# Optimization experiments

Hardware: AMD Instinct MI355X
Metric: run time of the kernel (lower is better)

The kernel has to match this reference:

```python
import jax, jax.numpy as jnp
import numpy as np

N = 8192          # tokens
D_IN = 32768      # dec_input_size (SAE latent dim)
D_OUT = 768       # dec_hidden_size (model resid dim)


def setup_inputs() -> dict:
    key = jax.random.key(0)
    kx, kw = jax.random.split(key)
    x = jax.random.normal(kx, (N, D_IN), dtype=jnp.float32)
    W = jax.random.normal(kw, (D_OUT, D_IN), dtype=jnp.float32) * (1.0 / np.sqrt(D_IN))
    b_pre = jnp.zeros((D_IN,), dtype=jnp.float32)
    return {"x": x, "W": W, "b_pre": b_pre}


def reference(x, W, b_pre):
    # x: [N, D_in]; subtract pre-bias, then dense decode: (x - b_pre) @ W^T -> [N, D_out]
    x_adj = x - b_pre
    return jnp.einsum('nd,od->no', x_adj, W)
```

## Files before the change

kernel.cpp:

```cpp
#include <hip/hip_runtime.h>
#include <hip/hip_bf16.h>

#define TOK 8192
#define OUTD 768
#define KD 32768

#define BM 128
#define BN 768
#define BK 32
#define SPLITK 4
#define KCHUNK (KD / SPLITK)
#define NKT (KCHUNK / BK)
#define NHT_TOT (KD / BK)
#define THREADS 512
#define HTILE (BN * BK * 2)
#define ATILE (BM * BK * 2)

#define WSOFF_W 4096
#define WSOFF_P (WSOFF_W + (long)NHT_TOT * HTILE)
#define PSTRIDE ((long)TOK * OUTD)

typedef __attribute__((ext_vector_type(4))) float f32x4;
typedef __attribute__((ext_vector_type(16))) float f32x16;
typedef __attribute__((ext_vector_type(8))) short bf16x8;
typedef __attribute__((ext_vector_type(4))) unsigned int u32x4;

__device__ __forceinline__ unsigned pack2(float lo, float hi) {
    __hip_bfloat162 h = __float22bfloat162_rn(make_float2(lo, hi));
    unsigned u;
    __builtin_memcpy(&u, &h, 4);
    return u;
}

__device__ __forceinline__ u32x4 cvt_chunk(f32x4 a, f32x4 b) {
    u32x4 r;
    r[0] = pack2(a[0], a[1]);
    r[1] = pack2(a[2], a[3]);
    r[2] = pack2(b[0], b[1]);
    r[3] = pack2(b[2], b[3]);
    return r;
}

__global__ void colbias_kernel(const float* __restrict__ W,
                               const float* __restrict__ bp,
                               float* __restrict__ negc) {
    int o = blockIdx.x;
    int tid = threadIdx.x;
    const float* wr = W + (long)o * KD;
    float s = 0.f;
    for (int i = tid * 4; i < KD; i += 256 * 4) {
        f32x4 w = *(const f32x4*)(wr + i);
        f32x4 b = *(const f32x4*)(bp + i);
        s += w[0] * b[0] + w[1] * b[1] + w[2] * b[2] + w[3] * b[3];
    }
    #pragma unroll
    for (int off = 32; off > 0; off >>= 1) s += __shfl_down(s, off);
    __shared__ float red[4];
    if ((tid & 63) == 0) red[tid >> 6] = s;
    __syncthreads();
    if (tid == 0) negc[o] = -(red[0] + red[1] + red[2] + red[3]);
}

__global__ void cast_w_kernel(const float* __restrict__ W,
                              char* __restrict__ wsW) {
    int kth = blockIdx.x;
    int tid = threadIdx.x;
    int q = tid & 3;
    int c0 = tid >> 2;
    #pragma unroll
    for (int i = 0; i < 6; ++i) {
        int c = c0 + i * 128;
        const float* src = W + (long)c * KD + kth * 32 + q * 8;
        f32x4 a = ((const f32x4*)src)[0];
        f32x4 b = ((const f32x4*)src)[1];
        char* dst = wsW + (long)kth * HTILE + c * 64 + ((q ^ (c & 3)) << 4);
        *(u32x4*)dst = cvt_chunk(a, b);
    }
}

__global__ __launch_bounds__(THREADS, 2) void decoder_gemm(
    const float* __restrict__ X, const char* __restrict__ Wb16,
    float* __restrict__ P) {
    __shared__ char lds[2 * ATILE + 2 * HTILE];
    char* ldsA = lds;
    char* ldsB = lds + 2 * ATILE;

    const int bid = blockIdx.x;
    const int ks = bid & (SPLITK - 1);
    const int mt = bid >> 2;
    const int row0 = mt * BM;

    const int tid = threadIdx.x;
    const int lane = tid & 63;
    const int wid = tid >> 6;
    const int wm = wid >> 2;
    const int wn = wid & 3;
    const int l31 = lane & 31;
    const int hi = lane >> 5;

    const float* Xb = X + (long)row0 * KD + (long)ks * KCHUNK;
    const char* Wt0 = Wb16 + (long)ks * NKT * HTILE;

    const int ar = tid >> 2;
    const int aq = tid & 3;
    f32x4 xr[2];

    auto LOADA = [&](int kt) {
        const f32x4* p = (const f32x4*)(Xb + (long)ar * KD + kt * 32 + aq * 8);
        xr[0] = p[0];
        xr[1] = p[1];
    };

    const int asoff = ar * 64 + ((aq ^ (ar & 3)) << 4);

    auto STOREA = [&](int buf) {
        *(u32x4*)(ldsA + buf * ATILE + asoff) = cvt_chunk(xr[0], xr[1]);
    };

    auto ISSUEB = [&](int kt, int buf) {
        const char* src = Wt0 + (long)kt * HTILE + tid * 16;
        char* dst = ldsB + buf * HTILE + tid * 16;
        #pragma unroll
        for (int j = 0; j < 6; ++j)
            __builtin_amdgcn_global_load_lds(
                (const __attribute__((address_space(1))) void*)(src + j * 8192),
                (__attribute__((address_space(3))) void*)(dst + j * 8192),
                16, 0, 0);
    };

    int aoff[2], boff[6];
    #pragma unroll
    for (int m = 0; m < 2; ++m) {
        int row = wm * 64 + m * 32 + l31;
        aoff[m] = row * 64 + ((hi ^ (row & 3)) << 4);
    }
    #pragma unroll
    for (int n = 0; n < 6; ++n) {
        int col = wn * 192 + n * 32 + l31;
        boff[n] = col * 64 + ((hi ^ (col & 3)) << 4);
    }

    f32x16 acc[2][6];
    #pragma unroll
    for (int m = 0; m < 2; ++m)
        #pragma unroll
        for (int n = 0; n < 6; ++n)
            #pragma unroll
            for (int r = 0; r < 16; ++r) acc[m][n][r] = 0.f;

    auto COMPUTE = [&](int cur) {
        const char* As = ldsA + cur * ATILE;
        const char* Bs = ldsB + cur * HTILE;
        #pragma unroll
        for (int kk = 0; kk < 2; ++kk) {
            bf16x8 afr[2], bfr[6];
            #pragma unroll
            for (int m = 0; m < 2; ++m)
                afr[m] = *(const bf16x8*)(As + (aoff[m] ^ (kk << 5)));
            #pragma unroll
            for (int n = 0; n < 6; ++n)
                bfr[n] = *(const bf16x8*)(Bs + (boff[n] ^ (kk << 5)));
            __builtin_amdgcn_s_setprio(1);
            #pragma unroll
            for (int m = 0; m < 2; ++m)
                #pragma unroll
                for (int n = 0; n < 6; ++n)
                    acc[m][n] = __builtin_amdgcn_mfma_f32_32x32x16_bf16(
                        afr[m], bfr[n], acc[m][n], 0, 0, 0);
            __builtin_amdgcn_s_setprio(0);
        }
    };

    ISSUEB(0, 0);
    LOADA(0);
    STOREA(0);
    __syncthreads();

    for (int kt = 0; kt < NKT; ++kt) {
        const int cur = kt & 1;
        const bool more = (kt + 1 < NKT);
        if (more) {
            ISSUEB(kt + 1, cur ^ 1);
            LOADA(kt + 1);
        }
        COMPUTE(cur);
        if (more) STOREA(cur ^ 1);
        __syncthreads();
    }

    float* Pk = P + (long)ks * PSTRIDE;
    #pragma unroll
    for (int m = 0; m < 2; ++m) {
        int rowb = row0 + wm * 64 + m * 32 + 4 * hi;
        #pragma unroll
        for (int n = 0; n < 6; ++n) {
            int col = wn * 192 + n * 32 + l31;
            #pragma unroll
            for (int r = 0; r < 16; ++r) {
                int row = rowb + (r & 3) + 8 * (r >> 2);
                Pk[(long)row * OUTD + col] = acc[m][n][r];
            }
        }
    }
}

__global__ void reduce_kernel(const float* __restrict__ P,
                              const float* __restrict__ negc,
                              float* __restrict__ out) {
    long i4 = ((long)blockIdx.x * blockDim.x + threadIdx.x) * 4;
    int col = (int)(i4 % OUTD);
    f32x4 s = *(const f32x4*)(negc + col);
    #pragma unroll
    for (int ks = 0; ks < SPLITK; ++ks)
        s += *(const f32x4*)(P + ks * PSTRIDE + i4);
    *(f32x4*)(out + i4) = s;
}

extern "C" void kernel_launch(void* const* d_in, const int* in_sizes, int n_in,
                              void* d_out, int out_size, void* d_ws,
                              size_t ws_size, hipStream_t stream) {
    const float* x = (const float*)d_in[0];
    const float* W = (const float*)d_in[1];
    const float* bp = (const float*)d_in[2];
    float* out = (float*)d_out;
    float* negc = (float*)d_ws;
    char* wsW = (char*)d_ws + WSOFF_W;
    float* wsP = (float*)((char*)d_ws + WSOFF_P);

    hipLaunchKernelGGL(colbias_kernel, dim3(OUTD), dim3(256), 0, stream, W, bp,
                       negc);
    hipLaunchKernelGGL(cast_w_kernel, dim3(NHT_TOT), dim3(512), 0, stream, W,
                       wsW);
    hipLaunchKernelGGL(decoder_gemm, dim3((TOK / BM) * SPLITK), dim3(THREADS),
                       0, stream, x, wsW, wsP);
    hipLaunchKernelGGL(reduce_kernel, dim3((TOK * OUTD) / (256 * 4)), dim3(256),
                       0, stream, wsP, negc, out);
}
```

Measured before the change: 574.7 us.

## Triple-buffer W tiles with single A buffer and explicit vmcnt waits

Replaces the double-buffered A/B pipeline with a three-stage ring for the bf16 W tiles, prefetched two k-steps ahead, and a single LDS buffer for the converted X tile. Uses explicit s_waitcnt vmcnt(6) so the newest B prefetch can stay in flight across the barrier, plus a second barrier before each A store. The aim is to hide more global-to-LDS latency of the large W tile behind MFMA work. Launch bounds drop to 1 block per SM, which allows more registers but risks lower occupancy and an extra barrier per iteration.

```diff
diff --git a/kernel.cpp b/kernel.cpp
--- a/kernel.cpp
+++ b/kernel.cpp
@@ -78,12 +78,12 @@
     }
 }
 
-__global__ __launch_bounds__(THREADS, 2) void decoder_gemm(
+__global__ __launch_bounds__(THREADS, 1) void decoder_gemm(
     const float* __restrict__ X, const char* __restrict__ Wb16,
     float* __restrict__ P) {
-    __shared__ char lds[2 * ATILE + 2 * HTILE];
+    __shared__ char lds[ATILE + 3 * HTILE];
     char* ldsA = lds;
-    char* ldsB = lds + 2 * ATILE;
+    char* ldsB = lds + ATILE;
 
     const int bid = blockIdx.x;
     const int ks = bid & (SPLITK - 1);
@@ -113,8 +113,8 @@
 
     const int asoff = ar * 64 + ((aq ^ (ar & 3)) << 4);
 
-    auto STOREA = [&](int buf) {
-        *(u32x4*)(ldsA + buf * ATILE + asoff) = cvt_chunk(xr[0], xr[1]);
+    auto STOREA = [&]() {
+        *(u32x4*)(ldsA + asoff) = cvt_chunk(xr[0], xr[1]);
     };
 
     auto ISSUEB = [&](int kt, int buf) {
@@ -148,9 +148,9 @@
             #pragma unroll
             for (int r = 0; r < 16; ++r) acc[m][n][r] = 0.f;
 
-    auto COMPUTE = [&](int cur) {
-        const char* As = ldsA + cur * ATILE;
-        const char* Bs = ldsB + cur * HTILE;
+    auto COMPUTE = [&](int bbuf) {
+        const char* As = ldsA;
+        const char* Bs = ldsB + bbuf * HTILE;
         #pragma unroll
         for (int kk = 0; kk < 2; ++kk) {
             bf16x8 afr[2], bfr[6];
@@ -171,21 +171,27 @@
         }
     };
 
+    LOADA(0);
     ISSUEB(0, 0);
-    LOADA(0);
-    STOREA(0);
-    __syncthreads();
+    STOREA();
+    ISSUEB(1, 1);
+    asm volatile("s_waitcnt vmcnt(6) lgkmcnt(0)" ::: "memory");
+    __builtin_amdgcn_sched_barrier(0);
+    __builtin_amdgcn_s_barrier();
 
     for (int kt = 0; kt < NKT; ++kt) {
-        const int cur = kt & 1;
-        const bool more = (kt + 1 < NKT);
-        if (more) {
-            ISSUEB(kt + 1, cur ^ 1);
-            LOADA(kt + 1);
+        if (kt + 1 < NKT) LOADA(kt + 1);
+        if (kt + 2 < NKT) ISSUEB(kt + 2, (kt + 2) % 3);
+        COMPUTE(kt % 3);
+        __builtin_amdgcn_s_barrier();
+        if (kt + 1 < NKT) STOREA();
+        if (kt + 2 < NKT) {
+            asm volatile("s_waitcnt vmcnt(6) lgkmcnt(0)" ::: "memory");
+        } else {
+            asm volatile("s_waitcnt vmcnt(0) lgkmcnt(0)" ::: "memory");
         }
-        COMPUTE(cur);
-        if (more) STOREA(cur ^ 1);
-        __syncthreads();
+        __builtin_amdgcn_sched_barrier(0);
+        __builtin_amdgcn_s_barrier();
     }
 
     float* Pk = P + (long)ks * PSTRIDE;
```

New measurement: 629.9 us. 9.6% more time.

## Load bf16 W fragments directly from global memory, drop LDS staging for B

Applied to the files above, without the earlier changes.

W is now cast to a plain row-major bf16 copy, and each lane reads its B fragments for the MFMA straight from global memory instead of staging the 768xBK tile through LDS. BK doubles to 64 and split-K doubles to 8. Only the x tile goes through LDS, now with an 8-way XOR swizzle. This removes the large B-tile LDS traffic and frees LDS, but puts global-load latency on the MFMA path without prefetch. It also doubles the partial-sum buffers written and read by the reduce kernel.

```diff
diff --git a/kernel.cpp b/kernel.cpp
--- a/kernel.cpp
+++ b/kernel.cpp
@@ -7,17 +7,15 @@
 
 #define BM 128
 #define BN 768
-#define BK 32
-#define SPLITK 4
+#define BK 64
+#define SPLITK 8
 #define KCHUNK (KD / SPLITK)
 #define NKT (KCHUNK / BK)
-#define NHT_TOT (KD / BK)
 #define THREADS 512
-#define HTILE (BN * BK * 2)
 #define ATILE (BM * BK * 2)
 
 #define WSOFF_W 4096
-#define WSOFF_P (WSOFF_W + (long)NHT_TOT * HTILE)
+#define WSOFF_P (WSOFF_W + (long)OUTD * KD * 2)
 #define PSTRIDE ((long)TOK * OUTD)
 
 typedef __attribute__((ext_vector_type(4))) float f32x4;
@@ -63,31 +61,27 @@
 
 __global__ void cast_w_kernel(const float* __restrict__ W,
                               char* __restrict__ wsW) {
-    int kth = blockIdx.x;
+    int col = blockIdx.x;
     int tid = threadIdx.x;
-    int q = tid & 3;
-    int c0 = tid >> 2;
-    #pragma unroll
-    for (int i = 0; i < 6; ++i) {
-        int c = c0 + i * 128;
-        const float* src = W + (long)c * KD + kth * 32 + q * 8;
-        f32x4 a = ((const f32x4*)src)[0];
-        f32x4 b = ((const f32x4*)src)[1];
-        char* dst = wsW + (long)kth * HTILE + c * 64 + ((q ^ (c & 3)) << 4);
-        *(u32x4*)dst = cvt_chunk(a, b);
+    const float* src = W + (long)col * KD;
+    char* dst = wsW + (long)col * KD * 2;
+    #pragma unroll
+    for (int i = 0; i < 16; ++i) {
+        int k = (tid + i * 256) * 8;
+        f32x4 a = *(const f32x4*)(src + k);
+        f32x4 b = *(const f32x4*)(src + k + 4);
+        *(u32x4*)(dst + k * 2) = cvt_chunk(a, b);
     }
 }
 
 __global__ __launch_bounds__(THREADS, 2) void decoder_gemm(
-    const float* __restrict__ X, const char* __restrict__ Wb16,
+    const float* __restrict__ X, const char* __restrict__ Wb,
     float* __restrict__ P) {
-    __shared__ char lds[2 * ATILE + 2 * HTILE];
-    char* ldsA = lds;
-    char* ldsB = lds + 2 * ATILE;
+    __shared__ char ldsA[2 * ATILE];
 
     const int bid = blockIdx.x;
     const int ks = bid & (SPLITK - 1);
-    const int mt = bid >> 2;
+    const int mt = bid >> 3;
     const int row0 = mt * BM;
 
     const int tid = threadIdx.x;
@@ -99,45 +93,41 @@
     const int hi = lane >> 5;
 
     const float* Xb = X + (long)row0 * KD + (long)ks * KCHUNK;
-    const char* Wt0 = Wb16 + (long)ks * NKT * HTILE;
+
+    const char* bptr[6];
+    #pragma unroll
+    for (int n = 0; n < 6; ++n) {
+        int col = wn * 192 + n * 32 + l31;
+        bptr[n] = Wb + ((long)col * KD + (long)ks * KCHUNK) * 2 + hi * 16;
+    }
 
     const int ar = tid >> 2;
     const int aq = tid & 3;
-    f32x4 xr[2];
+    f32x4 xr[4];
 
     auto LOADA = [&](int kt) {
-        const f32x4* p = (const f32x4*)(Xb + (long)ar * KD + kt * 32 + aq * 8);
+        const f32x4* p = (const f32x4*)(Xb + (long)ar * KD + kt * 64 + aq * 16);
         xr[0] = p[0];
         xr[1] = p[1];
+        xr[2] = p[2];
+        xr[3] = p[3];
     };
 
-    const int asoff = ar * 64 + ((aq ^ (ar & 3)) << 4);
+    const int soff1 = ar * 128 + (((aq * 2) ^ (ar & 7)) << 4);
+    const int soff2 = ar * 128 + (((aq * 2 + 1) ^ (ar & 7)) << 4);
 
     auto STOREA = [&](int buf) {
-        *(u32x4*)(ldsA + buf * ATILE + asoff) = cvt_chunk(xr[0], xr[1]);
+        char* base = ldsA + buf * ATILE;
+        *(u32x4*)(base + soff1) = cvt_chunk(xr[0], xr[1]);
+        *(u32x4*)(base + soff2) = cvt_chunk(xr[2], xr[3]);
     };
 
-    auto ISSUEB = [&](int kt, int buf) {
-        const char* src = Wt0 + (long)kt * HTILE + tid * 16;
-        char* dst = ldsB + buf * HTILE + tid * 16;
-        #pragma unroll
-        for (int j = 0; j < 6; ++j)
-            __builtin_amdgcn_global_load_lds(
-                (const __attribute__((address_space(1))) void*)(src + j * 8192),
-                (__attribute__((address_space(3))) void*)(dst + j * 8192),
-                16, 0, 0);
-    };
-
-    int aoff[2], boff[6];
+    int arow[2], arx[2];
     #pragma unroll
     for (int m = 0; m < 2; ++m) {
         int row = wm * 64 + m * 32 + l31;
-        aoff[m] = row * 64 + ((hi ^ (row & 3)) << 4);
-    }
-    #pragma unroll
-    for (int n = 0; n < 6; ++n) {
-        int col = wn * 192 + n * 32 + l31;
-        boff[n] = col * 64 + ((hi ^ (col & 3)) << 4);
+        arow[m] = row * 128;
+        arx[m] = row & 7;
     }
 
     f32x16 acc[2][6];
@@ -148,18 +138,20 @@
             #pragma unroll
             for (int r = 0; r < 16; ++r) acc[m][n][r] = 0.f;
 
-    auto COMPUTE = [&](int cur) {
-        const char* As = ldsA + cur * ATILE;
-        const char* Bs = ldsB + cur * HTILE;
+    auto COMPUTE = [&](int buf, int kt) {
+        const char* base = ldsA + buf * ATILE;
         #pragma unroll
-        for (int kk = 0; kk < 2; ++kk) {
-            bf16x8 afr[2], bfr[6];
-            #pragma unroll
-            for (int m = 0; m < 2; ++m)
-                afr[m] = *(const bf16x8*)(As + (aoff[m] ^ (kk << 5)));
+        for (int kk = 0; kk < 4; ++kk) {
+            bf16x8 bfr[6], afr[2];
             #pragma unroll
             for (int n = 0; n < 6; ++n)
-                bfr[n] = *(const bf16x8*)(Bs + (boff[n] ^ (kk << 5)));
+                bfr[n] = *(const bf16x8*)(bptr[n] + kt * 128 + kk * 32);
+            #pragma unroll
+            for (int m = 0; m < 2; ++m) {
+                int oct = kk * 2 + hi;
+                afr[m] = *(const bf16x8*)(base + arow[m] +
+                                          ((oct ^ arx[m]) << 4));
+            }
             __builtin_amdgcn_s_setprio(1);
             #pragma unroll
             for (int m = 0; m < 2; ++m)
@@ -171,7 +163,6 @@
         }
     };
 
-    ISSUEB(0, 0);
     LOADA(0);
     STOREA(0);
     __syncthreads();
@@ -179,11 +170,8 @@
     for (int kt = 0; kt < NKT; ++kt) {
         const int cur = kt & 1;
         const bool more = (kt + 1 < NKT);
-        if (more) {
-            ISSUEB(kt + 1, cur ^ 1);
-            LOADA(kt + 1);
-        }
-        COMPUTE(cur);
+        if (more) LOADA(kt + 1);
+        COMPUTE(cur, kt);
         if (more) STOREA(cur ^ 1);
         __syncthreads();
     }
@@ -229,7 +217,7 @@
 
     hipLaunchKernelGGL(colbias_kernel, dim3(OUTD), dim3(256), 0, stream, W, bp,
                        negc);
-    hipLaunchKernelGGL(cast_w_kernel, dim3(NHT_TOT), dim3(512), 0, stream, W,
+    hipLaunchKernelGGL(cast_w_kernel, dim3(OUTD), dim3(256), 0, stream, W,
                        wsW);
     hipLaunchKernelGGL(decoder_gemm, dim3((TOK / BM) * SPLITK), dim3(THREADS),
                        0, stream, x, wsW, wsP);
```

After: 1.311 ms. +128.0%, slower.

## Triple-buffer W tiles in LDS with prefetch distance two and lighter barriers

Applied to the files above, without the earlier changes.

The GEMM main loop now keeps three LDS buffers for the bf16 W tiles and issues the direct-to-LDS load two K-steps ahead, while X still uses double buffering. Each iteration ends with an explicit LDS-counter wait and raw s_barrier instead of __syncthreads, so the block no longer waits on all outstanding global loads. The aim is to hide more global-load latency behind the MFMA work. Correctness relies on the in-order vector-memory counter: the wait for the X register loads also forces the earlier W load to complete. LDS use rises to about 160 KB per block, which leaves no spare room and keeps one block per CU.

```diff
diff --git a/kernel.cpp b/kernel.cpp
--- a/kernel.cpp
+++ b/kernel.cpp
@@ -81,7 +81,7 @@
 __global__ __launch_bounds__(THREADS, 2) void decoder_gemm(
     const float* __restrict__ X, const char* __restrict__ Wb16,
     float* __restrict__ P) {
-    __shared__ char lds[2 * ATILE + 2 * HTILE];
+    __shared__ char lds[2 * ATILE + 3 * HTILE];
     char* ldsA = lds;
     char* ldsB = lds + 2 * ATILE;
 
@@ -148,9 +148,9 @@
             #pragma unroll
             for (int r = 0; r < 16; ++r) acc[m][n][r] = 0.f;
 
-    auto COMPUTE = [&](int cur) {
-        const char* As = ldsA + cur * ATILE;
-        const char* Bs = ldsB + cur * HTILE;
+    auto COMPUTE = [&](int b3, int abuf) {
+        const char* As = ldsA + abuf * ATILE;
+        const char* Bs = ldsB + b3 * HTILE;
         #pragma unroll
         for (int kk = 0; kk < 2; ++kk) {
             bf16x8 afr[2], bfr[6];
@@ -174,18 +174,23 @@
     ISSUEB(0, 0);
     LOADA(0);
     STOREA(0);
-    __syncthreads();
+    ISSUEB(1, 1);
+    asm volatile("s_waitcnt lgkmcnt(0)" ::: "memory");
+    __builtin_amdgcn_sched_barrier(0);
+    __builtin_amdgcn_s_barrier();
+    __builtin_amdgcn_sched_barrier(0);
 
     for (int kt = 0; kt < NKT; ++kt) {
-        const int cur = kt & 1;
-        const bool more = (kt + 1 < NKT);
-        if (more) {
-            ISSUEB(kt + 1, cur ^ 1);
-            LOADA(kt + 1);
-        }
-        COMPUTE(cur);
-        if (more) STOREA(cur ^ 1);
-        __syncthreads();
+        const bool moreA = (kt + 1 < NKT);
+        const bool moreB = (kt + 2 < NKT);
+        if (moreA) LOADA(kt + 1);
+        if (moreB) ISSUEB(kt + 2, (kt + 2) % 3);
+        COMPUTE(kt % 3, kt & 1);
+        if (moreA) STOREA((kt + 1) & 1);
+        asm volatile("s_waitcnt lgkmcnt(0)" ::: "memory");
+        __builtin_amdgcn_sched_barrier(0);
+        __builtin_amdgcn_s_barrier();
+        __builtin_amdgcn_sched_barrier(0);
     }
 
     float* Pk = P + (long)ks * PSTRIDE;
```

Measured after the change: 619.1 us. 7.7% more time.
